# Optimization experiments

Hardware: AMD Instinct MI355X
Metric: run time of the kernel (lower is better)

## Reference

```python
import jax, jax.numpy as jnp
import numpy as np

B, S, DIN = 2, 2048, 2048
H, G, D = 32, 8, 64  # num_heads, num_kv_groups, head_dim
GS = H // G          # group_size
EPS = 1e-6


def _rmsnorm(x, scale):
    # qwen3-compatible: compute in fp32, cast back
    xf = x.astype(jnp.float32)
    ms = jnp.mean(xf * xf, axis=-1, keepdims=True)
    return (xf * jax.lax.rsqrt(ms + EPS) * scale).astype(x.dtype)


def _rope(x, cos, sin):
    # x: [b, h, s, d]; cos/sin: [s, d]
    d2 = x.shape[-1] // 2
    x1, x2 = x[..., :d2], x[..., d2:]
    rotated = jnp.concatenate([-x2, x1], axis=-1)
    return (x * cos[None, None] + rotated * sin[None, None]).astype(x.dtype)


def setup_inputs() -> dict:
    key = jax.random.key(0)
    ks = jax.random.split(key, 8)
    x = jax.random.normal(ks[0], (B, S, DIN), dtype=jnp.float32)
    # causal mask: True = masked (future positions)
    mask = jnp.triu(jnp.ones((S, S), dtype=bool), k=1)
    # standard RoPE tables [S, D]
    inv_freq = 1.0 / (10000.0 ** (np.arange(0, D, 2, dtype=np.float32) / D))
    ang = np.arange(S, dtype=np.float32)[:, None] * inv_freq[None, :]
    ang = np.concatenate([ang, ang], axis=-1)  # [S, D]
    cos = jnp.asarray(np.cos(ang), dtype=jnp.float32)
    sin = jnp.asarray(np.sin(ang), dtype=jnp.float32)
    s = 0.02
    Wq = jax.random.normal(ks[1], (DIN, H * D), dtype=jnp.float32) * s
    Wk = jax.random.normal(ks[2], (DIN, G * D), dtype=jnp.float32) * s
    Wv = jax.random.normal(ks[3], (DIN, G * D), dtype=jnp.float32) * s
    Wo = jax.random.normal(ks[4], (H * D, DIN), dtype=jnp.float32) * s
    q_scale = jnp.ones((D,), dtype=jnp.float32)
    k_scale = jnp.ones((D,), dtype=jnp.float32)
    return dict(x=x, mask=mask, cos=cos, sin=sin, Wq=Wq, Wk=Wk, Wv=Wv, Wo=Wo,
                q_scale=q_scale, k_scale=k_scale)


def reference(x, mask, cos, sin, Wq, Wk, Wv, Wo, q_scale, k_scale):
    b, s, _ = x.shape
    # QKV projections -> [b, heads, s, D]
    q = (x @ Wq).reshape(b, s, H, D).transpose(0, 2, 1, 3)
    k = (x @ Wk).reshape(b, s, G, D).transpose(0, 2, 1, 3)
    v = (x @ Wv).reshape(b, s, G, D).transpose(0, 2, 1, 3)
    # qk RMSNorm (per-head-dim)
    q = _rmsnorm(q, q_scale)
    k = _rmsnorm(k, k_scale)
    # RoPE (start_pos=0, no cache)
    q = _rope(q, cos, sin)
    k = _rope(k, cos, sin)
    # GQA: group query heads instead of repeat_interleaving KV (same math)
    qg = q.reshape(b, G, GS, s, D)
    scores = jnp.einsum('bghqd,bgkd->bghqk', qg, k) / jnp.float32(np.sqrt(D))
    scores = jnp.where(mask[None, None, None], -jnp.inf, scores)
    w = jax.nn.softmax(scores, axis=-1)
    ctx = jnp.einsum('bghqk,bgkd->bghqd', w, v)
    ctx = ctx.reshape(b, H, s, D).transpose(0, 2, 1, 3).reshape(b, s, H * D)
    out = ctx @ Wo
    return out, (k, v)
```

## Files before the change

### kernel.cpp

```cpp
#include <hip/hip_runtime.h>

typedef __bf16 bf16_t;
typedef bf16_t bf16x8 __attribute__((ext_vector_type(8)));
typedef float f32x4 __attribute__((ext_vector_type(4)));

#define MFMA16(a, b, c) __builtin_amdgcn_mfma_f32_16x16x32_bf16(a, b, c, 0, 0, 0)

__device__ __forceinline__ unsigned short f2bf(float f) {
    union { float f; unsigned u; } v; v.f = f;
    unsigned r = v.u + 0x7FFFu + ((v.u >> 16) & 1u);
    return (unsigned short)(r >> 16);
}
__device__ __forceinline__ float bf2f(unsigned short h) {
    union { unsigned u; float f; } v; v.u = ((unsigned)h) << 16;
    return v.f;
}
__device__ __forceinline__ unsigned short to_bf(float f) {
    bf16_t b = (bf16_t)f;
    return __builtin_bit_cast(unsigned short, b);
}

__device__ __forceinline__ void gll16(const unsigned short* g, unsigned short* l) {
    __builtin_amdgcn_global_load_lds(
        (const __attribute__((address_space(1))) unsigned int*)g,
        (__attribute__((address_space(3))) unsigned int*)l, 16, 0, 0);
}

__global__ __launch_bounds__(256) void cast_x_kernel(const float* __restrict__ src,
                                                     unsigned short* __restrict__ dst, int n) {
    int i = (blockIdx.x * 256 + threadIdx.x) * 4;
    if (i >= n) return;
    float4 v = *(const float4*)&src[i];
    union { unsigned short e[4]; uint2 u; } p;
    p.e[0] = f2bf(v.x); p.e[1] = f2bf(v.y); p.e[2] = f2bf(v.z); p.e[3] = f2bf(v.w);
    *(uint2*)&dst[i] = p.u;
}

__global__ __launch_bounds__(256) void castT_kernel(const float* __restrict__ src,
                                                    unsigned short* __restrict__ dst,
                                                    int N) {
    __shared__ __align__(16) unsigned short sT[64 * 68];
    int nt = blockIdx.x >> 5;
    int kt = blockIdx.x & 31;
    int k0 = kt * 64, n0 = nt * 64;
    int t = threadIdx.x;
#pragma unroll
    for (int c = t; c < 1024; c += 256) {
        int r = c >> 4, c4 = c & 15;
        float4 v = *(const float4*)&src[(size_t)(k0 + r) * N + n0 + c4 * 4];
        union { unsigned short e[4]; uint2 u; } p;
        p.e[0] = f2bf(v.x); p.e[1] = f2bf(v.y); p.e[2] = f2bf(v.z); p.e[3] = f2bf(v.w);
        *(uint2*)&sT[r * 68 + c4 * 4] = p.u;
    }
    __syncthreads();
#pragma unroll
    for (int c = t; c < 512; c += 256) {
        int n = c >> 3, cb = c & 7;
        union { unsigned short e[8]; uint4 v; } u;
#pragma unroll
        for (int j = 0; j < 8; ++j) u.e[j] = sT[(cb * 8 + j) * 68 + n];
        *(uint4*)&dst[(size_t)(n0 + n) * 2048 + k0 + cb * 8] = u.v;
    }
}

__global__ __launch_bounds__(512) void gemm256_bt(
    const unsigned short* __restrict__ A,
    const unsigned short* __restrict__ Bt,
    float* __restrict__ Cf, unsigned short* __restrict__ Cb,
    int M, int N, int K)
{
    extern __shared__ unsigned short lds[];
    const int KT = K >> 6;
    const int NIT = KT >> 1;

    int tid = threadIdx.x;
    int lane = tid & 63, w = tid >> 6;
    int wmi = w >> 2, wni = w & 3;
    int lo = lane & 15, quad = lane >> 4;
    int m0 = blockIdx.y * 256, n0 = blockIdx.x * 256;

    int rsub = lane >> 3;
    int csw  = ((lane & 7) ^ rsub) << 3;

    f32x4 acc[8][4];
#pragma unroll
    for (int i = 0; i < 8; ++i)
#pragma unroll
        for (int j = 0; j < 4; ++j) acc[i][j] = (f32x4){0.f, 0.f, 0.f, 0.f};

    auto stA = [&](int buf, int mp, int T) {
#pragma unroll
        for (int j = 0; j < 2; ++j) {
            int rr = (w * 2 + j) * 8 + rsub;
            gll16(A + (size_t)(m0 + mp * 128 + rr) * K + T * 64 + csw,
                  lds + buf * 32768 + mp * 8192 + (w * 2 + j) * 512);
        }
    };
    auto stB = [&](int buf, int np, int T) {
#pragma unroll
        for (int j = 0; j < 2; ++j) {
            int rr = (w * 2 + j) * 8 + rsub;
            gll16(Bt + (size_t)(n0 + np * 128 + rr) * K + T * 64 + csw,
                  lds + buf * 32768 + 16384 + np * 8192 + (w * 2 + j) * 512);
        }
    };

    auto phase = [&](int buf, int mp, int np, auto stage, bool drain) {
        bf16x8 a[4][2], b2[2][2];
#pragma unroll
        for (int mf = 0; mf < 4; ++mf)
#pragma unroll
            for (int k2 = 0; k2 < 2; ++k2) {
                int r = mp * 128 + wmi * 64 + mf * 16 + lo;
                int u = quad + k2 * 4;
                a[mf][k2] = *(const bf16x8*)&lds[buf * 32768 + r * 64 + ((u ^ (lo & 7)) << 3)];
            }
#pragma unroll
        for (int nf = 0; nf < 2; ++nf)
#pragma unroll
            for (int k2 = 0; k2 < 2; ++k2) {
                int r = np * 128 + wni * 32 + nf * 16 + lo;
                int u = quad + k2 * 4;
                b2[nf][k2] = *(const bf16x8*)&lds[buf * 32768 + 16384 + r * 64 + ((u ^ (lo & 7)) << 3)];
            }
        stage();
        __builtin_amdgcn_s_barrier();
        __builtin_amdgcn_sched_barrier(0);
        __builtin_amdgcn_s_setprio(1);
#pragma unroll
        for (int mf = 0; mf < 4; ++mf)
#pragma unroll
            for (int nf = 0; nf < 2; ++nf) {
                f32x4 z = acc[mp * 4 + mf][np * 2 + nf];
                z = MFMA16(a[mf][0], b2[nf][0], z);
                z = MFMA16(a[mf][1], b2[nf][1], z);
                acc[mp * 4 + mf][np * 2 + nf] = z;
            }
        __builtin_amdgcn_s_setprio(0);
        if (drain) asm volatile("s_waitcnt vmcnt(0)" ::: "memory");
        else       asm volatile("s_waitcnt vmcnt(6)" ::: "memory");
        __builtin_amdgcn_s_barrier();
        __builtin_amdgcn_sched_barrier(0);
    };
    auto nop = [&] {};

    stA(0, 0, 0); stB(0, 0, 0); stA(0, 1, 0); stB(0, 1, 0);
    stA(1, 0, 1); stB(1, 0, 1);
    asm volatile("s_waitcnt vmcnt(4)" ::: "memory");
    __builtin_amdgcn_s_barrier();
    __builtin_amdgcn_sched_barrier(0);

    for (int i = 0; i < NIT - 1; ++i) {
        int T1 = 2 * i + 1, T2 = 2 * i + 2, T3 = 2 * i + 3;
        phase(0, 0, 0, [&] { stA(1, 1, T1); }, false);
        phase(0, 0, 1, [&] { stB(1, 1, T1); }, false);
        phase(0, 1, 0, [&] { stA(0, 0, T2); }, false);
        phase(0, 1, 1, [&] { stB(0, 0, T2); }, false);
        phase(1, 0, 0, [&] { stA(0, 1, T2); }, false);
        phase(1, 0, 1, [&] { stB(0, 1, T2); }, false);
        phase(1, 1, 0, [&] { stA(1, 0, T3); }, false);
        phase(1, 1, 1, [&] { stB(1, 0, T3); }, false);
    }
    {
        int T1 = KT - 1;
        phase(0, 0, 0, [&] { stA(1, 1, T1); }, false);
        phase(0, 0, 1, [&] { stB(1, 1, T1); }, true);
        phase(0, 1, 0, nop, false);
        phase(0, 1, 1, nop, false);
        phase(1, 0, 0, nop, false);
        phase(1, 0, 1, nop, false);
        phase(1, 1, 0, nop, false);
        phase(1, 1, 1, nop, false);
    }

#pragma unroll
    for (int mi = 0; mi < 8; ++mi) {
        int mp = mi >> 2, mf = mi & 3;
        int row_base = m0 + mp * 128 + wmi * 64 + mf * 16 + quad * 4;
#pragma unroll
        for (int ni = 0; ni < 4; ++ni) {
            int np = ni >> 1, nf = ni & 1;
            int col = n0 + np * 128 + wni * 32 + nf * 16 + lo;
#pragma unroll
            for (int r = 0; r < 4; ++r) {
                int row = row_base + r;
                if (Cf) Cf[(size_t)row * N + col] = acc[mi][ni][r];
                else    Cb[(size_t)row * N + col] = f2bf(acc[mi][ni][r]);
            }
        }
    }
}

__global__ __launch_bounds__(256) void rmsrope_kernel(
    const unsigned short* __restrict__ qkv,
    const float* __restrict__ cosb, const float* __restrict__ sinb,
    const float* __restrict__ q_scale, const float* __restrict__ k_scale,
    unsigned short* __restrict__ q_attn, unsigned short* __restrict__ k_attn,
    float* __restrict__ k_out, float* __restrict__ v_out)
{
    int wid = blockIdx.x * 4 + (threadIdx.x >> 6);
    int lane = threadIdx.x & 63;
    int t = wid % 48;
    int bs = wid / 48;
    int b = bs >> 11, s = bs & 2047;

    if (t >= 40) {
        int g = t - 40;
        float val = bf2f(qkv[(size_t)bs * 3072 + 2560 + g * 64 + lane]);
        v_out[(size_t)((b * 8 + g) * 2048 + s) * 64 + lane] = val;
        return;
    }
    bool is_q = (t < 32);
    int col = is_q ? (t * 64) : (2048 + (t - 32) * 64);
    float val = bf2f(qkv[(size_t)bs * 3072 + col + lane]);
    float ss = val * val;
#pragma unroll
    for (int m = 1; m < 64; m <<= 1) ss += __shfl_xor(ss, m);
    float rs = rsqrtf(ss * (1.0f / 64.0f) + 1e-6f);
    float scl = is_q ? q_scale[lane] : k_scale[lane];
    float xn = val * rs * scl;
    float other = __shfl_xor(xn, 32);
    float rot = (lane < 32) ? -other : other;
    float o = xn * cosb[s * 64 + lane] + rot * sinb[s * 64 + lane];
    if (is_q) {
        q_attn[(size_t)((b * 32 + t) * 2048 + s) * 64 + lane] = to_bf(o * (0.125f * 1.44269504f));
    } else {
        int g = t - 32;
        size_t idx = (size_t)((b * 8 + g) * 2048 + s) * 64 + lane;
        k_attn[idx] = to_bf(o);
        k_out[idx] = o;
    }
}

__global__ __launch_bounds__(256) void vtrans_kernel(
    const unsigned short* __restrict__ qkv, unsigned short* __restrict__ vt)
{
    __shared__ __align__(16) unsigned short sT[64 * 68];
    int idx = blockIdx.x;
    int st = idx & 31, g = (idx >> 5) & 7, b = idx >> 8;
    int tid = threadIdx.x;
#pragma unroll
    for (int c = tid; c < 512; c += 256) {
        int r = c >> 3, cb = c & 7;
        *(uint4*)&sT[r * 68 + cb * 8] =
            *(const uint4*)&qkv[(size_t)(b * 2048 + st * 64 + r) * 3072 + 2560 + g * 64 + cb * 8];
    }
    __syncthreads();
#pragma unroll
    for (int c = tid; c < 512; c += 256) {
        int d = c >> 3, cb = c & 7;
        union { unsigned short e[8]; uint4 v; } u;
#pragma unroll
        for (int j = 0; j < 8; ++j) u.e[j] = sT[(cb * 8 + j) * 68 + d];
        *(uint4*)&vt[((size_t)(b * 8 + g) * 64 + d) * 2048 + st * 64 + cb * 8] = u.v;
    }
}

__global__ __launch_bounds__(256, 2) void attn_kernel(
    const unsigned short* __restrict__ q_attn,
    const unsigned short* __restrict__ k_attn,
    const unsigned short* __restrict__ vt,
    unsigned short* __restrict__ ctx)
{
    __shared__ __align__(16) unsigned short sK[2][4096];
    __shared__ __align__(16) unsigned short sV[2][4096];
    __shared__ __align__(16) unsigned short sP[4][16 * 68];

    int w = threadIdx.x >> 6;
    int lane = threadIdx.x & 63;

    int g = blockIdx.x & 7;
    int ord = blockIdx.x >> 3;
    int b = ord & 1;
    int qt = 63 - (ord >> 1);
    int h = g * 4 + w;

    int lo = lane & 15, quad = lane >> 4;
    unsigned short* sPw = sP[w];

    const unsigned short* Qb = q_attn + (size_t)(b * 32 + h) * 2048 * 64;
    const unsigned short* Kb = k_attn + (size_t)(b * 8 + g) * 2048 * 64;
    const unsigned short* Vb = vt + (size_t)(b * 8 + g) * 64 * 2048;

    int nt = (qt >> 1) + 1;

    int rsub = lane >> 3;
    int csw  = ((lane & 7) ^ rsub) << 3;

    auto STAGE = [&](int buf, int kt) {
#pragma unroll
        for (int i = 0; i < 2; ++i) {
            int c = w + i * 4;
            gll16(Kb + (size_t)(kt * 64 + c * 8 + rsub) * 64 + csw, &sK[buf][c * 512]);
            gll16(Vb + (size_t)(c * 8 + rsub) * 2048 + kt * 64 + csw, &sV[buf][c * 512]);
        }
    };

    const bf16_t one = (bf16_t)1.0f;
    const bf16x8 vone = {one, one, one, one, one, one, one, one};

    bf16x8 qf[2][2];
#pragma unroll
    for (int mt = 0; mt < 2; ++mt)
#pragma unroll
        for (int h2 = 0; h2 < 2; ++h2)
            qf[mt][h2] = *(const bf16x8*)&Qb[(size_t)(qt * 32 + mt * 16 + lo) * 64 + h2 * 32 + quad * 8];

    f32x4 o_acc[2][4];
    f32x4 l_acc[2];
#pragma unroll
    for (int mt = 0; mt < 2; ++mt) {
        l_acc[mt] = (f32x4){0.f, 0.f, 0.f, 0.f};
#pragma unroll
        for (int j = 0; j < 4; ++j) o_acc[mt][j] = (f32x4){0.f, 0.f, 0.f, 0.f};
    }

    STAGE(0, 0);
    __syncthreads();

    int cur = 0;
    for (int kt = 0; kt < nt; ++kt) {
        if (kt + 1 < nt) STAGE(cur ^ 1, kt + 1);

        const char* sKc = (const char*)sK[cur];
        const char* sVc = (const char*)sV[cur];
        bool domask = (kt == nt - 1);

#pragma unroll
        for (int mt = 0; mt < 2; ++mt) {
            f32x4 sc[4];
            __builtin_amdgcn_s_setprio(1);
#pragma unroll
            for (int ct = 0; ct < 4; ++ct) {
                int krow = ct * 16 + lo;
                int rsw = (krow & 7) << 4;
                bf16x8 kf0 = *(const bf16x8*)(sKc + (krow << 7) + (((quad << 4)) ^ rsw));
                bf16x8 kf1 = *(const bf16x8*)(sKc + (krow << 7) + (((1 << 6) | (quad << 4)) ^ rsw));
                f32x4 z = (f32x4){0.f, 0.f, 0.f, 0.f};
                z = MFMA16(qf[mt][0], kf0, z);
                z = MFMA16(qf[mt][1], kf1, z);
                sc[ct] = z;
            }
            __builtin_amdgcn_s_setprio(0);
            if (domask) {
                int qrow0 = qt * 32 + mt * 16 + quad * 4;
#pragma unroll
                for (int ct = 0; ct < 4; ++ct)
#pragma unroll
                    for (int r = 0; r < 4; ++r)
                        if (kt * 64 + ct * 16 + lo > qrow0 + r) sc[ct][r] = -INFINITY;
            }
#pragma unroll
            for (int ct = 0; ct < 4; ++ct)
#pragma unroll
                for (int r = 0; r < 4; ++r)
                    sc[ct][r] = __builtin_amdgcn_exp2f(sc[ct][r]);

#pragma unroll
            for (int ct = 0; ct < 4; ++ct)
#pragma unroll
                for (int r = 0; r < 4; ++r)
                    sPw[(quad * 4 + r) * 68 + ct * 16 + lo] = to_bf(sc[ct][r]);

            bf16x8 pf0 = *(const bf16x8*)&sPw[lo * 68 + quad * 8];
            bf16x8 pf1 = *(const bf16x8*)&sPw[lo * 68 + 32 + quad * 8];

            __builtin_amdgcn_s_setprio(1);
            l_acc[mt] = MFMA16(pf0, vone, l_acc[mt]);
            l_acc[mt] = MFMA16(pf1, vone, l_acc[mt]);

#pragma unroll
            for (int nt2 = 0; nt2 < 4; ++nt2) {
                int vrow = nt2 * 16 + lo;
                int rsw = (vrow & 7) << 4;
                bf16x8 vf0 = *(const bf16x8*)(sVc + (vrow << 7) + (((quad << 4)) ^ rsw));
                bf16x8 vf1 = *(const bf16x8*)(sVc + (vrow << 7) + (((1 << 6) | (quad << 4)) ^ rsw));
                f32x4 oo = o_acc[mt][nt2];
                oo = MFMA16(pf0, vf0, oo);
                oo = MFMA16(pf1, vf1, oo);
                o_acc[mt][nt2] = oo;
            }
            __builtin_amdgcn_s_setprio(0);
        }

        __syncthreads();
        cur ^= 1;
    }

#pragma unroll
    for (int mt = 0; mt < 2; ++mt)
#pragma unroll
        for (int r = 0; r < 4; ++r) {
            float inv = 1.0f / l_acc[mt][r];
            int row = qt * 32 + mt * 16 + quad * 4 + r;
#pragma unroll
            for (int nt2 = 0; nt2 < 4; ++nt2) {
                size_t oi = ((size_t)(b * 2048 + row)) * 2048 + h * 64 + nt2 * 16 + lo;
                ctx[oi] = to_bf(o_acc[mt][nt2][r] * inv);
            }
        }
}

extern "C" void kernel_launch(void* const* d_in, const int* in_sizes, int n_in,
                              void* d_out, int out_size, void* d_ws, size_t ws_size,
                              hipStream_t stream)
{
    (void)in_sizes; (void)n_in; (void)out_size; (void)ws_size;
    const float* x       = (const float*)d_in[0];
    const float* cosb    = (const float*)d_in[2];
    const float* sinb    = (const float*)d_in[3];
    const float* Wq      = (const float*)d_in[4];
    const float* Wk      = (const float*)d_in[5];
    const float* Wv      = (const float*)d_in[6];
    const float* Wo      = (const float*)d_in[7];
    const float* q_scale = (const float*)d_in[8];
    const float* k_scale = (const float*)d_in[9];

    float* out   = (float*)d_out;
    float* k_out = out + 8388608;
    float* v_out = k_out + 2097152;

    static bool attr_done = false;
    if (!attr_done) {
        hipFuncSetAttribute((const void*)gemm256_bt,
                            hipFuncAttributeMaxDynamicSharedMemorySize, 131072);
        attr_done = true;
    }

    char* ws = (char*)d_ws;
    size_t off = 0;
    auto alloc = [&](size_t bytes) {
        char* p = ws + off; off += (bytes + 255) & ~(size_t)255; return p;
    };
    unsigned short* x_bf   = (unsigned short*)alloc(4096ull * 2048 * 2);
    unsigned short* Wqkvt  = (unsigned short*)alloc(3072ull * 2048 * 2);
    unsigned short* Wot    = (unsigned short*)alloc(2048ull * 2048 * 2);
    unsigned short* qkv    = (unsigned short*)alloc(4096ull * 3072 * 2);
    unsigned short* q_attn = (unsigned short*)alloc(4096ull * 2048 * 2);
    unsigned short* k_attn = (unsigned short*)alloc(2048ull * 2048 * 2);
    unsigned short* vt     = (unsigned short*)alloc(2097152ull * 2);
    unsigned short* ctx    = (unsigned short*)alloc(4096ull * 2048 * 2);

    cast_x_kernel<<<8192, 256, 0, stream>>>(x, x_bf, 8388608);
    castT_kernel<<<1024, 256, 0, stream>>>(Wq, Wqkvt, 2048);
    castT_kernel<<<256, 256, 0, stream>>>(Wk, Wqkvt + 2048ull * 2048, 512);
    castT_kernel<<<256, 256, 0, stream>>>(Wv, Wqkvt + 2560ull * 2048, 512);
    castT_kernel<<<1024, 256, 0, stream>>>(Wo, Wot, 2048);

    gemm256_bt<<<dim3(12, 16), 512, 131072, stream>>>(x_bf, Wqkvt, nullptr, qkv, 4096, 3072, 2048);

    rmsrope_kernel<<<49152, 256, 0, stream>>>(qkv, cosb, sinb, q_scale, k_scale,
                                              q_attn, k_attn, k_out, v_out);
    vtrans_kernel<<<512, 256, 0, stream>>>(qkv, vt);

    attn_kernel<<<1024, 256, 0, stream>>>(q_attn, k_attn, vt, ctx);

    gemm256_bt<<<dim3(8, 16), 512, 131072, stream>>>(ctx, Wot, out, nullptr, 4096, 2048, 2048);
}
```

Before: 396.2 us.

## Use 256x128 GEMM tiles for output projection and merge weight-cast launches

```diff
diff --git a/kernel.cpp b/kernel.cpp
--- a/kernel.cpp
+++ b/kernel.cpp
@@ -36,12 +36,20 @@
     *(uint2*)&dst[i] = p.u;
 }
 
-__global__ __launch_bounds__(256) void castT_kernel(const float* __restrict__ src,
-                                                    unsigned short* __restrict__ dst,
-                                                    int N) {
+__global__ __launch_bounds__(256) void castT_all_kernel(
+    const float* __restrict__ Wq, const float* __restrict__ Wk,
+    const float* __restrict__ Wv, const float* __restrict__ Wo,
+    unsigned short* __restrict__ Wqkvt, unsigned short* __restrict__ Wot)
+{
     __shared__ __align__(16) unsigned short sT[64 * 68];
-    int nt = blockIdx.x >> 5;
-    int kt = blockIdx.x & 31;
+    int idx = blockIdx.x;
+    const float* src; unsigned short* dst; int N; int loc;
+    if (idx < 1024)      { src = Wq; dst = Wqkvt;                    N = 2048; loc = idx; }
+    else if (idx < 1280) { src = Wk; dst = Wqkvt + 2048ull * 2048;   N = 512;  loc = idx - 1024; }
+    else if (idx < 1536) { src = Wv; dst = Wqkvt + 2560ull * 2048;   N = 512;  loc = idx - 1280; }
+    else                 { src = Wo; dst = Wot;                      N = 2048; loc = idx - 1536; }
+    int nt = loc >> 5;
+    int kt = loc & 31;
     int k0 = kt * 64, n0 = nt * 64;
     int t = threadIdx.x;
 #pragma unroll
@@ -186,6 +194,121 @@
                 int row = row_base + r;
                 if (Cf) Cf[(size_t)row * N + col] = acc[mi][ni][r];
                 else    Cb[(size_t)row * N + col] = f2bf(acc[mi][ni][r]);
+            }
+        }
+    }
+}
+
+__global__ __launch_bounds__(512) void gemm256x128_bt(
+    const unsigned short* __restrict__ A,
+    const unsigned short* __restrict__ Bt,
+    float* __restrict__ Cf, unsigned short* __restrict__ Cb,
+    int M, int N, int K)
+{
+    extern __shared__ unsigned short lds[];
+    const int KT = K >> 6;
+    const int NIT = KT >> 1;
+
+    int tid = threadIdx.x;
+    int lane = tid & 63, w = tid >> 6;
+    int wmi = w >> 2, wni = w & 3;
+    int lo = lane & 15, quad = lane >> 4;
+    int m0 = blockIdx.y * 256, n0 = blockIdx.x * 128;
+
+    int rsub = lane >> 3;
+    int csw  = ((lane & 7) ^ rsub) << 3;
+
+    f32x4 acc[8][2];
+#pragma unroll
+    for (int i = 0; i < 8; ++i)
+#pragma unroll
+        for (int j = 0; j < 2; ++j) acc[i][j] = (f32x4){0.f, 0.f, 0.f, 0.f};
+
+    auto stA = [&](int d, int u, int T) {
+        int Tc = T >= KT ? T - KT : T;
+#pragma unroll
+        for (int j = 0; j < 2; ++j) {
+            int rr = u * 128 + (w * 2 + j) * 8 + rsub;
+            gll16(A + (size_t)(m0 + rr) * K + Tc * 64 + csw,
+                  lds + d * 16384 + u * 8192 + (w * 2 + j) * 512);
+        }
+    };
+    auto stB = [&](int T) {
+        int t3 = T % 3;
+        int Tc = T >= KT ? T - KT : T;
+#pragma unroll
+        for (int j = 0; j < 2; ++j) {
+            int rr = (w * 2 + j) * 8 + rsub;
+            gll16(Bt + (size_t)(n0 + rr) * K + Tc * 64 + csw,
+                  lds + 32768 + t3 * 8192 + (w * 2 + j) * 512);
+        }
+    };
+
+    auto phase = [&](int d, int t3, int mp, auto stage, bool w8) {
+        bf16x8 a[4][2], b2[2][2];
+#pragma unroll
+        for (int mf = 0; mf < 4; ++mf)
+#pragma unroll
+            for (int k2 = 0; k2 < 2; ++k2) {
+                int r = mp * 128 + wmi * 64 + mf * 16 + lo;
+                int u = quad + k2 * 4;
+                a[mf][k2] = *(const bf16x8*)&lds[d * 16384 + r * 64 + ((u ^ (lo & 7)) << 3)];
+            }
+#pragma unroll
+        for (int nf = 0; nf < 2; ++nf)
+#pragma unroll
+            for (int k2 = 0; k2 < 2; ++k2) {
+                int r = wni * 32 + nf * 16 + lo;
+                int u = quad + k2 * 4;
+                b2[nf][k2] = *(const bf16x8*)&lds[32768 + t3 * 8192 + r * 64 + ((u ^ (lo & 7)) << 3)];
+            }
+        stage();
+        __builtin_amdgcn_s_barrier();
+        __builtin_amdgcn_sched_barrier(0);
+        __builtin_amdgcn_s_setprio(1);
+#pragma unroll
+        for (int mf = 0; mf < 4; ++mf)
+#pragma unroll
+            for (int nf = 0; nf < 2; ++nf) {
+                f32x4 z = acc[mp * 4 + mf][nf];
+                z = MFMA16(a[mf][0], b2[nf][0], z);
+                z = MFMA16(a[mf][1], b2[nf][1], z);
+                acc[mp * 4 + mf][nf] = z;
+            }
+        __builtin_amdgcn_s_setprio(0);
+        if (w8) asm volatile("s_waitcnt vmcnt(8)" ::: "memory");
+        else    asm volatile("s_waitcnt vmcnt(6)" ::: "memory");
+        __builtin_amdgcn_s_barrier();
+        __builtin_amdgcn_sched_barrier(0);
+    };
+
+    stA(0, 0, 0); stA(0, 1, 0); stB(0);
+    stA(1, 0, 1); stB(1);
+    asm volatile("s_waitcnt vmcnt(4)" ::: "memory");
+    __builtin_amdgcn_s_barrier();
+    __builtin_amdgcn_sched_barrier(0);
+
+    for (int i = 0; i < NIT; ++i) {
+        int T0 = 2 * i, T1 = 2 * i + 1, T2 = 2 * i + 2, T3 = 2 * i + 3;
+        int b0 = T0 % 3, b1 = T1 % 3;
+        phase(0, b0, 0, [&] { stA(1, 1, T1); stB(T2); }, true);
+        phase(0, b0, 1, [&] { stA(0, 0, T2); },          false);
+        phase(1, b1, 0, [&] { stA(0, 1, T2); stB(T3); }, true);
+        phase(1, b1, 1, [&] { stA(1, 0, T3); },          false);
+    }
+
+#pragma unroll
+    for (int mi = 0; mi < 8; ++mi) {
+        int mp = mi >> 2, mf = mi & 3;
+        int row_base = m0 + mp * 128 + wmi * 64 + mf * 16 + quad * 4;
+#pragma unroll
+        for (int nf = 0; nf < 2; ++nf) {
+            int col = n0 + wni * 32 + nf * 16 + lo;
+#pragma unroll
+            for (int r = 0; r < 4; ++r) {
+                int row = row_base + r;
+                if (Cf) Cf[(size_t)row * N + col] = acc[mi][nf][r];
+                else    Cb[(size_t)row * N + col] = f2bf(acc[mi][nf][r]);
             }
         }
     }
@@ -424,6 +547,8 @@
     if (!attr_done) {
         hipFuncSetAttribute((const void*)gemm256_bt,
                             hipFuncAttributeMaxDynamicSharedMemorySize, 131072);
+        hipFuncSetAttribute((const void*)gemm256x128_bt,
+                            hipFuncAttributeMaxDynamicSharedMemorySize, 114688);
         attr_done = true;
     }
 
@@ -442,10 +567,7 @@
     unsigned short* ctx    = (unsigned short*)alloc(4096ull * 2048 * 2);
 
     cast_x_kernel<<<8192, 256, 0, stream>>>(x, x_bf, 8388608);
-    castT_kernel<<<1024, 256, 0, stream>>>(Wq, Wqkvt, 2048);
-    castT_kernel<<<256, 256, 0, stream>>>(Wk, Wqkvt + 2048ull * 2048, 512);
-    castT_kernel<<<256, 256, 0, stream>>>(Wv, Wqkvt + 2560ull * 2048, 512);
-    castT_kernel<<<1024, 256, 0, stream>>>(Wo, Wot, 2048);
+    castT_all_kernel<<<2560, 256, 0, stream>>>(Wq, Wk, Wv, Wo, Wqkvt, Wot);
 
     gemm256_bt<<<dim3(12, 16), 512, 131072, stream>>>(x_bf, Wqkvt, nullptr, qkv, 4096, 3072, 2048);
 
@@ -455,5 +577,5 @@
 
     attn_kernel<<<1024, 256, 0, stream>>>(q_attn, k_attn, vt, ctx);
 
-    gemm256_bt<<<dim3(8, 16), 512, 131072, stream>>>(ctx, Wot, out, nullptr, 4096, 2048, 2048);
-}
+    gemm256x128_bt<<<dim3(16, 16), 512, 114688, stream>>>(ctx, Wot, out, nullptr, 4096, 2048, 2048);
+}
```

Result: faster. 361.4 us (-8.8%).
